# Performance work log

Hardware: AMD Instinct MI355X
Metric: run time of the kernel (lower is better)

## Reference

```python
import jax, jax.numpy as jnp
import numpy as np

T, IN_SZ, OUT_SZ = 512, 1024, 1024
INIT_TAU = 2.0   # sig_tau = sigmoid(init_tau) is the leak factor
V_TH = 1.0


def setup_inputs() -> dict:
    key = jax.random.key(0)
    k1, k2 = jax.random.split(key)
    x_seq = jax.random.normal(k1, (T, IN_SZ), jnp.float32)
    kernel = jax.random.normal(k2, (IN_SZ, OUT_SZ), jnp.float32) / np.float32(np.sqrt(IN_SZ))
    u0 = jnp.zeros((OUT_SZ,), jnp.float32)
    E0 = jnp.zeros((IN_SZ, OUT_SZ), jnp.float32)  # eligibility trace, same shape as kernel
    return {"x_seq": x_seq, "kernel": kernel, "u0": u0, "E0": E0}


def reference(x_seq, kernel, u0, E0):
    # Forward pass of the OSTL-wrapped spiking cell over a sequence.
    # Primal path (f): LIF dynamics with soft reset; E is not touched in primal.
    sig_tau = jax.nn.sigmoid(jnp.float32(INIT_TAU))
    vth = jnp.float32(V_TH)

    def body(u, x):
        u_new = sig_tau * u + x @ kernel          # [OUT_SZ]
        s = (u_new > vth).astype(x.dtype)          # heaviside spike
        u_out = u_new - s * vth                    # soft reset
        return u_out, s

    u_final, spikes = jax.lax.scan(body, u0, x_seq)  # spikes: [T, OUT_SZ]
    return spikes, u_final
```

## Files before the change

kernel.cpp:

```cpp
#include <hip/hip_runtime.h>
#include <stdint.h>


#define T_STEPS 512
#define IN_SZ   1024
#define OUT_SZ  1024

#define BM 128
#define BN 128
#define BK 32
#define KSPLIT 8
#define KCHUNK (IN_SZ / KSPLIT)
#define NITER  (KCHUNK / BK)

typedef __attribute__((address_space(1))) const void gvoid;
typedef __attribute__((address_space(3))) void lvoid;

__global__ __launch_bounds__(256) void ostl_gemm_splitk(const float* __restrict__ X,
                                                        const float* __restrict__ W,
                                                        float* __restrict__ P) {
    __shared__ float As[2][BK][BM];
    __shared__ float Bs[2][BK * BN];

    const int tid = threadIdx.x;
    const int tx = tid & 15;
    const int ty = tid >> 4;
    const int n0 = blockIdx.x * BN;
    const int m0 = blockIdx.y * BM;
    const int kc = blockIdx.z;
    const int kb = kc * KCHUNK;

    const int am = tid >> 1;
    const int ak = (tid & 1) * 16;
    const int wv = tid >> 6;
    const int ln = tid & 63;

    const float* Arow = X + (size_t)(m0 + am) * IN_SZ + kb + ak;

    float4 areg[4];

    #pragma unroll
    for (int q = 0; q < 4; ++q)
        areg[q] = *reinterpret_cast<const float4*>(Arow + q * 4);
    #pragma unroll
    for (int j = 0; j < 4; ++j) {
        const int i = wv * 4 + j;
        const float* src = W + (size_t)(kb + 2 * i + (ln >> 5)) * OUT_SZ + n0 + (ln & 31) * 4;
        __builtin_amdgcn_global_load_lds((gvoid*)src, (lvoid*)&Bs[0][i * 256], 16, 0, 0);
    }
    {
        float t[16];
        #pragma unroll
        for (int q = 0; q < 4; ++q) *reinterpret_cast<float4*>(&t[q * 4]) = areg[q];
        #pragma unroll
        for (int c = 0; c < 16; ++c) As[0][ak + c][am] = t[c];
    }
    __syncthreads();

    float acc[8][8];
    #pragma unroll
    for (int r = 0; r < 8; ++r)
        #pragma unroll
        for (int c = 0; c < 8; ++c) acc[r][c] = 0.f;

    #pragma unroll 1
    for (int it = 0; it < NITER; ++it) {
        const int cur = it & 1;
        const int nxt = cur ^ 1;

        if (it < NITER - 1) {
            const int kbase = kb + (it + 1) * BK;
            #pragma unroll
            for (int j = 0; j < 4; ++j) {
                const int i = wv * 4 + j;
                const float* src = W + (size_t)(kbase + 2 * i + (ln >> 5)) * OUT_SZ + n0 + (ln & 31) * 4;
                __builtin_amdgcn_global_load_lds((gvoid*)src, (lvoid*)&Bs[nxt][i * 256], 16, 0, 0);
            }
            #pragma unroll
            for (int q = 0; q < 4; ++q)
                areg[q] = *reinterpret_cast<const float4*>(Arow + (it + 1) * BK + q * 4);
        }

        #pragma unroll 8
        for (int k = 0; k < BK; ++k) {
            const float4 a0 = *reinterpret_cast<const float4*>(&As[cur][k][ty * 8]);
            const float4 a1 = *reinterpret_cast<const float4*>(&As[cur][k][ty * 8 + 4]);
            const float4 b0 = *reinterpret_cast<const float4*>(&Bs[cur][k * BN + tx * 4]);
            const float4 b1 = *reinterpret_cast<const float4*>(&Bs[cur][k * BN + tx * 4 + 64]);
            const float av[8] = {a0.x, a0.y, a0.z, a0.w, a1.x, a1.y, a1.z, a1.w};
            const float bv[8] = {b0.x, b0.y, b0.z, b0.w, b1.x, b1.y, b1.z, b1.w};
            #pragma unroll
            for (int r = 0; r < 8; ++r)
                #pragma unroll
                for (int c = 0; c < 8; ++c)
                    acc[r][c] = fmaf(av[r], bv[c], acc[r][c]);
        }

        if (it < NITER - 1) {
            float t[16];
            #pragma unroll
            for (int q = 0; q < 4; ++q) *reinterpret_cast<float4*>(&t[q * 4]) = areg[q];
            #pragma unroll
            for (int c = 0; c < 16; ++c) As[nxt][ak + c][am] = t[c];
            __syncthreads();
        }
    }

    float* Pb = P + (size_t)kc * T_STEPS * OUT_SZ + (size_t)(m0 + ty * 8) * OUT_SZ + n0;
    #pragma unroll
    for (int r = 0; r < 8; ++r) {
        *reinterpret_cast<float4*>(&Pb[(size_t)r * OUT_SZ + tx * 4]) =
            make_float4(acc[r][0], acc[r][1], acc[r][2], acc[r][3]);
        *reinterpret_cast<float4*>(&Pb[(size_t)r * OUT_SZ + tx * 4 + 64]) =
            make_float4(acc[r][4], acc[r][5], acc[r][6], acc[r][7]);
    }
}

__device__ inline float4 f4add(float4 a, float4 b) {
    return make_float4(a.x + b.x, a.y + b.y, a.z + b.z, a.w + b.w);
}

__global__ __launch_bounds__(256) void ostl_reduce8(const float* __restrict__ P,
                                                    float* __restrict__ Y) {
    const size_t idx = ((size_t)blockIdx.x * 256 + threadIdx.x) * 4;
    float4 s[8];
    #pragma unroll
    for (int c = 0; c < 8; ++c)
        s[c] = *reinterpret_cast<const float4*>(P + (size_t)c * T_STEPS * OUT_SZ + idx);
    const float4 t0 = f4add(s[0], s[1]);
    const float4 t1 = f4add(s[2], s[3]);
    const float4 t2 = f4add(s[4], s[5]);
    const float4 t3 = f4add(s[6], s[7]);
    *reinterpret_cast<float4*>(Y + idx) = f4add(f4add(t0, t1), f4add(t2, t3));
}

__global__ __launch_bounds__(64) void ostl_scan_rl(const float* __restrict__ u0,
                                                   const float* __restrict__ Y,
                                                   unsigned* __restrict__ Bits,
                                                   float* __restrict__ u_final) {
    const int j = blockIdx.x;
    const int l = threadIdx.x;

    const float sig_f = (float)0.8807970779778823;

    float u = u0[j];
    unsigned sbits = 0u;

    float ycur = Y[(size_t)l * OUT_SZ + j];
    #pragma unroll 1
    for (int q = 0; q < 8; ++q) {
        float ynext = 0.f;
        if (q < 7)
            ynext = Y[(size_t)((q + 1) * 64 + l) * OUT_SZ + j];
        const unsigned qbit = 1u << q;
        #pragma unroll
        for (int i = 0; i < 64; ++i) {
            const float yv = __int_as_float(
                __builtin_amdgcn_readlane(__float_as_int(ycur), i));
            const float un = fmaf(sig_f, u, yv);
            const float us = un - 1.0f;
            const bool  sp = un > 1.0f;
            sbits |= (i == l && sp) ? qbit : 0u;
            u = sp ? us : un;
        }
        ycur = ynext;
    }
    Bits[(size_t)j * 64 + l] = sbits;
    if (l == 0) u_final[j] = u;
}

__global__ __launch_bounds__(256) void ostl_expand(const unsigned* __restrict__ Bits,
                                                   float* __restrict__ S) {
    const int t = blockIdx.x;
    const int c = t & 63;
    const int q = t >> 6;
    const int j4 = threadIdx.x * 4;
    float4 v;
    v.x = (float)((Bits[(size_t)(j4 + 0) * 64 + c] >> q) & 1u);
    v.y = (float)((Bits[(size_t)(j4 + 1) * 64 + c] >> q) & 1u);
    v.z = (float)((Bits[(size_t)(j4 + 2) * 64 + c] >> q) & 1u);
    v.w = (float)((Bits[(size_t)(j4 + 3) * 64 + c] >> q) & 1u);
    *reinterpret_cast<float4*>(&S[(size_t)t * OUT_SZ + j4]) = v;
}

extern "C" void kernel_launch(void* const* d_in, const int* in_sizes, int n_in,
                              void* d_out, int out_size, void* d_ws, size_t ws_size,
                              hipStream_t stream) {
    const float* x_seq  = (const float*)d_in[0];
    const float* kernel = (const float*)d_in[1];
    const float* u0     = (const float*)d_in[2];

    float* out      = (float*)d_out;
    float* spikes   = out;
    float* u_final  = out + (size_t)T_STEPS * OUT_SZ;

    float*    partials = (float*)d_ws;
    float*    yb       = partials + (size_t)KSPLIT * T_STEPS * OUT_SZ;
    unsigned* bits     = (unsigned*)(yb + (size_t)T_STEPS * OUT_SZ);

    dim3 ggrid(OUT_SZ / BN, T_STEPS / BM, KSPLIT);
    ostl_gemm_splitk<<<ggrid, dim3(256), 0, stream>>>(x_seq, kernel, partials);

    ostl_reduce8<<<dim3((T_STEPS * OUT_SZ / 4) / 256), dim3(256), 0, stream>>>(partials, yb);

    ostl_scan_rl<<<dim3(OUT_SZ), dim3(64), 0, stream>>>(u0, yb, bits, u_final);

    ostl_expand<<<dim3(T_STEPS), dim3(256), 0, stream>>>(bits, spikes);
}
```

Baseline: 106.9 us.

## Fuse split-K reduction and spike expansion into the scan kernel

Removes the separate reduce and expand kernels. The scan kernel now sums the eight split-K partials itself while it loads each 64-step chunk, and writes float spikes straight to the output instead of packing bits for a later pass. This saves two launches and the intermediate Y and bit buffers. In exchange, the scan's loads are 8x more numerous and strided by OUT_SZ (uncoalesced, one column per block), and its stores are scattered single floats per column, which risks poor memory efficiency.

```diff
diff --git a/kernel.cpp b/kernel.cpp
--- a/kernel.cpp
+++ b/kernel.cpp
@@ -116,43 +116,38 @@
     }
 }
 
-__device__ inline float4 f4add(float4 a, float4 b) {
-    return make_float4(a.x + b.x, a.y + b.y, a.z + b.z, a.w + b.w);
-}
-
-__global__ __launch_bounds__(256) void ostl_reduce8(const float* __restrict__ P,
-                                                    float* __restrict__ Y) {
-    const size_t idx = ((size_t)blockIdx.x * 256 + threadIdx.x) * 4;
-    float4 s[8];
-    #pragma unroll
-    for (int c = 0; c < 8; ++c)
-        s[c] = *reinterpret_cast<const float4*>(P + (size_t)c * T_STEPS * OUT_SZ + idx);
-    const float4 t0 = f4add(s[0], s[1]);
-    const float4 t1 = f4add(s[2], s[3]);
-    const float4 t2 = f4add(s[4], s[5]);
-    const float4 t3 = f4add(s[6], s[7]);
-    *reinterpret_cast<float4*>(Y + idx) = f4add(f4add(t0, t1), f4add(t2, t3));
-}
-
-__global__ __launch_bounds__(64) void ostl_scan_rl(const float* __restrict__ u0,
-                                                   const float* __restrict__ Y,
-                                                   unsigned* __restrict__ Bits,
-                                                   float* __restrict__ u_final) {
+__global__ __launch_bounds__(64) void ostl_scan_direct(const float* __restrict__ u0,
+                                                       const float* __restrict__ P,
+                                                       float* __restrict__ Sout,
+                                                       float* __restrict__ u_final) {
     const int j = blockIdx.x;
     const int l = threadIdx.x;
+    const size_t CS = (size_t)T_STEPS * OUT_SZ;
 
     const float sig_f = (float)0.8807970779778823;
 
     float u = u0[j];
-    unsigned sbits = 0u;
 
-    float ycur = Y[(size_t)l * OUT_SZ + j];
+    float ycur;
+    {
+        float raw[8];
+        #pragma unroll
+        for (int c = 0; c < 8; ++c)
+            raw[c] = P[c * CS + (size_t)l * OUT_SZ + j];
+        const float t0 = raw[0] + raw[1], t1 = raw[2] + raw[3];
+        const float t2 = raw[4] + raw[5], t3 = raw[6] + raw[7];
+        ycur = (t0 + t1) + (t2 + t3);
+    }
+
     #pragma unroll 1
     for (int q = 0; q < 8; ++q) {
-        float ynext = 0.f;
-        if (q < 7)
-            ynext = Y[(size_t)((q + 1) * 64 + l) * OUT_SZ + j];
-        const unsigned qbit = 1u << q;
+        float rawn[8];
+        if (q < 7) {
+            #pragma unroll
+            for (int c = 0; c < 8; ++c)
+                rawn[c] = P[c * CS + (size_t)((q + 1) * 64 + l) * OUT_SZ + j];
+        }
+        float spk = 0.f;
         #pragma unroll
         for (int i = 0; i < 64; ++i) {
             const float yv = __int_as_float(
@@ -160,27 +155,17 @@
             const float un = fmaf(sig_f, u, yv);
             const float us = un - 1.0f;
             const bool  sp = un > 1.0f;
-            sbits |= (i == l && sp) ? qbit : 0u;
+            if (i == l) spk = sp ? 1.0f : 0.0f;
             u = sp ? us : un;
         }
-        ycur = ynext;
+        Sout[(size_t)(q * 64 + l) * OUT_SZ + j] = spk;
+        if (q < 7) {
+            const float t0 = rawn[0] + rawn[1], t1 = rawn[2] + rawn[3];
+            const float t2 = rawn[4] + rawn[5], t3 = rawn[6] + rawn[7];
+            ycur = (t0 + t1) + (t2 + t3);
+        }
     }
-    Bits[(size_t)j * 64 + l] = sbits;
     if (l == 0) u_final[j] = u;
-}
-
-__global__ __launch_bounds__(256) void ostl_expand(const unsigned* __restrict__ Bits,
-                                                   float* __restrict__ S) {
-    const int t = blockIdx.x;
-    const int c = t & 63;
-    const int q = t >> 6;
-    const int j4 = threadIdx.x * 4;
-    float4 v;
-    v.x = (float)((Bits[(size_t)(j4 + 0) * 64 + c] >> q) & 1u);
-    v.y = (float)((Bits[(size_t)(j4 + 1) * 64 + c] >> q) & 1u);
-    v.z = (float)((Bits[(size_t)(j4 + 2) * 64 + c] >> q) & 1u);
-    v.w = (float)((Bits[(size_t)(j4 + 3) * 64 + c] >> q) & 1u);
-    *reinterpret_cast<float4*>(&S[(size_t)t * OUT_SZ + j4]) = v;
 }
 
 extern "C" void kernel_launch(void* const* d_in, const int* in_sizes, int n_in,
@@ -194,16 +179,10 @@
     float* spikes   = out;
     float* u_final  = out + (size_t)T_STEPS * OUT_SZ;
 
-    float*    partials = (float*)d_ws;
-    float*    yb       = partials + (size_t)KSPLIT * T_STEPS * OUT_SZ;
-    unsigned* bits     = (unsigned*)(yb + (size_t)T_STEPS * OUT_SZ);
+    float* partials = (float*)d_ws;
 
     dim3 ggrid(OUT_SZ / BN, T_STEPS / BM, KSPLIT);
     ostl_gemm_splitk<<<ggrid, dim3(256), 0, stream>>>(x_seq, kernel, partials);
 
-    ostl_reduce8<<<dim3((T_STEPS * OUT_SZ / 4) / 256), dim3(256), 0, stream>>>(partials, yb);
-
-    ostl_scan_rl<<<dim3(OUT_SZ), dim3(64), 0, stream>>>(u0, yb, bits, u_final);
-
-    ostl_expand<<<dim3(T_STEPS), dim3(256), 0, stream>>>(bits, spikes);
+    ostl_scan_direct<<<dim3(OUT_SZ), dim3(64), 0, stream>>>(u0, partials, spikes, u_final);
 }
```

After: 124.9 us. 1.17x slower.
